# Kernel tuning notes

Hardware: AMD Instinct MI355X
Metric: run time of the kernel (lower is better)

Reference implementation:

```python
import jax, jax.numpy as jnp
import numpy as np

V, C, L, D = 16384, 16, 6, 64  # n_vars, max_clauses, max_variables, embedding_dim


def _normalize(x):
    # utils.normalize: L2-normalize along the feature axis
    return x / jnp.linalg.norm(x, axis=-1, keepdims=True)


def _rescombine(x, W1, b1, W2, b2):
    # ResidualCombine: normalize(sigmoid(layer1(x)) + layer2(x))
    h = jax.nn.sigmoid(x @ W1 + b1) + x @ W2 + b2
    return _normalize(h)


def setup_inputs() -> dict:
    key = jax.random.key(0)
    ks = jax.random.split(key, 14)
    s = 0.05
    variables = jax.random.normal(ks[0], (V, D), jnp.float32)
    # literal variable indices; slot 0 of every clause is the owning variable i
    lits = jax.random.randint(ks[1], (V, C, L), 0, V)
    lits = lits.at[:, :, 0].set(jnp.arange(V)[:, None])
    neg_mask = jax.random.bernoulli(ks[2], 0.5, (V, C, L))
    # literal validity: at least 2 literals per clause, slot 0 always valid
    nvar = jax.random.randint(ks[3], (V, C), 2, L + 1)
    var_valid = jnp.arange(L)[None, None, :] < nvar[:, :, None]
    # clause validity: at least 1 clause per variable
    nclause = jax.random.randint(ks[4], (V,), 1, C + 1)
    clause_valid = jnp.arange(C)[None, :] < nclause[:, None]
    # params
    Wn = jax.random.normal(ks[5], (D, D), jnp.float32) * s
    bn = jnp.zeros((D,), jnp.float32)
    f = jax.random.normal(ks[6], (D,), jnp.float32)
    false_emb = f / jnp.linalg.norm(f)  # Embedding(1, D, max_norm=1.0)
    W1v = jax.random.normal(ks[7], (L * D, D), jnp.float32) * s
    b1v = jnp.zeros((D,), jnp.float32)
    W2v = jax.random.normal(ks[8], (L * D, D), jnp.float32) * s
    b2v = jnp.zeros((D,), jnp.float32)
    W1c = jax.random.normal(ks[9], (C * D, D), jnp.float32) * s
    b1c = jnp.zeros((D,), jnp.float32)
    W2c = jax.random.normal(ks[10], (C * D, D), jnp.float32) * s
    b2c = jnp.zeros((D,), jnp.float32)
    return dict(variables=variables, lits=lits, neg_mask=neg_mask, var_valid=var_valid,
                clause_valid=clause_valid, Wn=Wn, bn=bn, false_emb=false_emb,
                W1v=W1v, b1v=b1v, W2v=W2v, b2v=b2v, W1c=W1c, b1c=b1c, W2c=W2c, b2c=b2c)


def reference(variables, lits, neg_mask, var_valid, clause_valid,
              Wn, bn, false_emb, W1v, b1v, W2v, b2v, W1c, b1c, W2c, b2c):
    # gather literal embeddings: [V, C, L, D]
    g = variables[lits]
    # negation linear for negative literals
    v = jnp.where(neg_mask[..., None], g @ Wn + bn, g)
    # pad invalid literal slots with the 'false' embedding
    v = jnp.where(var_valid[..., None], v, false_emb)
    # variable_combiner over flattened [L*D]
    clause_emb = _rescombine(v.reshape(V, C, L * D), W1v, b1v, W2v, b2v)  # [V, C, D]
    # pad missing clauses with 'true' = negation(false)
    true_emb = false_emb @ Wn + bn
    clause_emb = jnp.where(clause_valid[..., None], clause_emb, true_emb)
    # clause_combiner over flattened [C*D]
    out = _rescombine(clause_emb.reshape(V, C * D), W1c, b1c, W2c, b2c)  # [V, D]
    # variables with no clauses pass through unchanged
    has_clauses = clause_valid.any(axis=-1)
    return jnp.where(has_clauses[:, None], out, variables)
```

## Files before the change

### kernel.cpp

```cpp
#include <hip/hip_runtime.h>
#include <hip/hip_bf16.h>

#define NV 16384
#define NC 16
#define NL 6
#define ND 64

typedef unsigned short u16;
typedef unsigned int u32;
typedef __attribute__((ext_vector_type(8))) short short8;
typedef __attribute__((ext_vector_type(4))) unsigned short u16x4;
typedef __attribute__((ext_vector_type(4))) int i32x4;
typedef __attribute__((ext_vector_type(4))) float f32x4;

#define PB_BN  0
#define PB_FE  64
#define PB_B1V 128
#define PB_B2V 192
#define PB_B1C 256
#define PB_B2C 320
#define U_BVS   896
#define U_BCS   50048
#define U_BN    181120
#define U_VARSB 185216
#define U_NEGB  1233856
#define U_FIDX  2282496

__device__ __forceinline__ float ldbf(const u16* p, int i) {
  return __uint_as_float(((u32)p[i]) << 16);
}
__device__ __forceinline__ u16 f2b(float f) {
  u32 x = __float_as_uint(f);
  return (u16)((x + 0x7FFF + ((x >> 16) & 1)) >> 16);
}
__device__ __forceinline__ int ldmask(const void* p, int i, int bdt) {
  return bdt ? (int)((const signed char*)p)[i] : ((const int*)p)[i];
}
__device__ __forceinline__ int ldmask_nt(const void* p, int i, int bdt) {
  return bdt ? (int)__builtin_nontemporal_load((const signed char*)p + i)
             : __builtin_nontemporal_load((const int*)p + i);
}
__device__ __forceinline__ float ldf(const void* p, int i, int fdt) {
  return fdt ? ldbf((const u16*)p, i) : ((const float*)p)[i];
}
__device__ __forceinline__ void gll16(const u16* g, u16* l) {
  __builtin_amdgcn_global_load_lds(
      (const __attribute__((address_space(1))) u32*)(g),
      (__attribute__((address_space(3))) u32*)(l), 16, 0, 0);
}

__global__ __launch_bounds__(256) void k_prep(
    const void* vars, const int* __restrict__ lits, const void* negm, const void* vval,
    const void* Wn, const void* bn, const void* femb,
    const void* W1v, const void* b1v, const void* W2v, const void* b2v,
    const void* W1c, const void* b1c, const void* W2c, const void* b2c,
    int* flags, float* pbuf, u16* wsB) {
  __shared__ int s_cnt[4], s_big[4];
  __shared__ u16 wn[64 * 72];
  const int t = threadIdx.x;
  {
    const u32 w = ((const u32*)vars)[t];
    const u32 e = (w >> 7) & 0xFF;
    const unsigned long long bal = __ballot(e >= 0x6E && e <= 0x8E);
    const u32 bw = ((const u32*)vval)[t];
    const unsigned long long bb = __ballot(bw > 1u);
    if ((t & 63) == 0) { s_cnt[t >> 6] = __popcll(bal); s_big[t >> 6] = (bb != 0ull); }
  }
  __syncthreads();
  const int fdt = (s_cnt[0] + s_cnt[1] + s_cnt[2] + s_cnt[3]) >= 192;
  const int bdt = (s_big[0] | s_big[1] | s_big[2] | s_big[3]);
  const int bid = blockIdx.x;

  if (bid == 0) {
    if (t == 0) { flags[0] = fdt; flags[1] = bdt; }
    if (t < 64) {
      const void* src[6] = {bn, femb, b1v, b2v, b1c, b2c};
      const int off[6] = {PB_BN, PB_FE, PB_B1V, PB_B2V, PB_B1C, PB_B2C};
      for (int j = 0; j < 6; j++) pbuf[off[j] + t] = ldf(src[j], t, fdt);
      wsB[U_VARSB + NV * 64 + t] = fdt ? ((const u16*)femb)[t] : f2b(((const float*)femb)[t]);
    }
  } else if (bid < 25) {
    const int c = (bid - 1) * 256 + t;
    const int ln = c & 63, nt = (c >> 6) & 7, ks = c >> 9;
    const int n = nt * 16 + (ln & 15);
    const void* src = (n < 64) ? W1v : W2v;
    const int kb = ks * 32 + (ln >> 4) * 8, n6 = n & 63;
    u16 o[8];
#pragma unroll
    for (int j = 0; j < 8; j++) o[j] = f2b(ldf(src, (kb + j) * 64 + n6, fdt));
    *(short8*)(wsB + U_BVS + c * 8) = *(short8*)o;
  } else if (bid < 89) {
    const int c = (bid - 25) * 256 + t;
    const int ln = c & 63, nt = (c >> 6) & 7, ks = c >> 9;
    const int n = nt * 16 + (ln & 15);
    const void* src = (n < 64) ? W1c : W2c;
    const int kb = ks * 32 + (ln >> 4) * 8, n6 = n & 63;
    u16 o[8];
#pragma unroll
    for (int j = 0; j < 8; j++) o[j] = f2b(ldf(src, (kb + j) * 64 + n6, fdt));
    *(short8*)(wsB + U_BCS + c * 8) = *(short8*)o;
  } else if (bid < 601) {
    const int c8 = (bid - 89) * 256 + t;
    u16 o[8];
    if (fdt) {
      *(short8*)o = ((const short8*)vars)[c8];
    } else {
      const float* f = (const float*)vars + c8 * 8;
#pragma unroll
      for (int j = 0; j < 8; j++) o[j] = f2b(f[j]);
    }
    *(short8*)(wsB + U_VARSB + c8 * 8) = *(short8*)o;
  } else if (bid < 1369) {
    const int i0 = ((bid - 601) * 256 + t) * 8;
    const i32x4 l0 = __builtin_nontemporal_load((const i32x4*)((const int*)lits + i0));
    const i32x4 l1 = __builtin_nontemporal_load((const i32x4*)((const int*)lits + i0) + 1);
    int nm[8], vv[8];
    if (bdt) {
      const unsigned long long nmq =
          __builtin_nontemporal_load((const unsigned long long*)((const signed char*)negm + i0));
      const unsigned long long vvq =
          __builtin_nontemporal_load((const unsigned long long*)((const signed char*)vval + i0));
#pragma unroll
      for (int j = 0; j < 8; j++) {
        nm[j] = (int)((nmq >> (8 * j)) & 0xFF);
        vv[j] = (int)((vvq >> (8 * j)) & 0xFF);
      }
    } else {
      const i32x4 n0 = __builtin_nontemporal_load((const i32x4*)((const int*)negm + i0));
      const i32x4 n1 = __builtin_nontemporal_load((const i32x4*)((const int*)negm + i0) + 1);
      const i32x4 v0 = __builtin_nontemporal_load((const i32x4*)((const int*)vval + i0));
      const i32x4 v1 = __builtin_nontemporal_load((const i32x4*)((const int*)vval + i0) + 1);
#pragma unroll
      for (int j = 0; j < 4; j++) {
        nm[j] = n0[j]; nm[4 + j] = n1[j];
        vv[j] = v0[j]; vv[4 + j] = v1[j];
      }
    }
    u16 o[8];
#pragma unroll
    for (int j = 0; j < 8; j++) {
      const int idx = (j < 4) ? l0[j] : l1[j - 4];
      o[j] = (u16)(vv[j] ? (idx + (nm[j] ? (NV + 1) : 0)) : NV);
    }
    __builtin_nontemporal_store(*(short8*)o, (short8*)(wsB + U_FIDX + i0));
  } else {
    const int nb = bid - 1369;
    for (int e = t; e < 4096; e += 256) {
      const int k = e >> 6, n = e & 63;
      wn[n * 72 + k] = f2b(ldf(Wn, e, fdt));
    }
    __syncthreads();
    const int lane = t & 63, wv = t >> 6;
    const int col = lane & 15, quad = lane >> 4, q8 = quad * 8;
    const int rowbase = nb * 64 + wv * 16;
    f32x4 acc[4];
#pragma unroll
    for (int nt = 0; nt < 4; nt++) acc[nt] = (f32x4){0.f, 0.f, 0.f, 0.f};
    const int arow = min(rowbase + col, NV);
#pragma unroll
    for (int ks = 0; ks < 2; ks++) {
      short8 a;
      if (fdt) {
        const u16* ap = (arow == NV) ? (const u16*)femb : (const u16*)vars + arow * 64;
        a = *(const short8*)(ap + ks * 32 + q8);
      } else {
        const float* ap = (arow == NV) ? (const float*)femb : (const float*)vars + arow * 64;
        const f32x4 f0 = *(const f32x4*)(ap + ks * 32 + q8);
        const f32x4 f1 = *(const f32x4*)(ap + ks * 32 + q8 + 4);
#pragma unroll
        for (int j = 0; j < 4; j++) { a[j] = (short)f2b(f0[j]); a[4 + j] = (short)f2b(f1[j]); }
      }
#pragma unroll
      for (int nt = 0; nt < 4; nt++) {
        const short8 b = *(const short8*)(&wn[(nt * 16 + col) * 72 + ks * 32 + q8]);
        acc[nt] = __builtin_amdgcn_mfma_f32_16x16x32_bf16(a, b, acc[nt], 0, 0, 0);
      }
    }
#pragma unroll
    for (int reg = 0; reg < 4; reg++) {
      const int r = rowbase + quad * 4 + reg;
      if (r <= NV) {
#pragma unroll
        for (int nt = 0; nt < 4; nt++) {
          const int d = nt * 16 + col;
          wsB[U_NEGB + r * 64 + d] = f2b(acc[nt][reg] + ldf(bn, d, fdt));
        }
      }
    }
  }
}

__global__ __launch_bounds__(256, 2) void k_main(
    const void* __restrict__ vars, const void* __restrict__ cval,
    const float* __restrict__ pbuf, const int* __restrict__ flags,
    const u16* __restrict__ wsB, void* __restrict__ outv) {
  __shared__ __align__(16) u16 smem[24576];
  __shared__ float ps[16][4];
  __shared__ int hcS[16];

  const int tid = threadIdx.x, lane = tid & 63, wv = tid >> 6;
  const int col = lane & 15, quad = lane >> 4, q8 = quad * 8;
  const int fdt = flags[0], bdt = flags[1];
  const int vbase = (blockIdx.x * 4 + wv) * 4;
  const int v0 = blockIdx.x * 16;

  u32 r2_[4][3];
#pragma unroll
  for (int v4 = 0; v4 < 4; v4++)
#pragma unroll
    for (int i = 0; i < 3; i++)
      r2_[v4][i] = __builtin_nontemporal_load(
          (const u32*)(wsB + U_FIDX + (vbase + v4) * 96 + col * 6 + i * 2));

  const int cv = ldmask_nt(cval, vbase * 16 + lane, bdt);
  const unsigned long long bal = __ballot(cv != 0);
  if (lane < 4) hcS[wv * 4 + lane] = ((bal >> (lane * 16)) & 0xFFFFull) != 0;

  f32x4 acc[4][8];
#pragma unroll
  for (int v4 = 0; v4 < 4; v4++)
#pragma unroll
    for (int nt = 0; nt < 8; nt++) acc[v4][nt] = (f32x4){0.f, 0.f, 0.f, 0.f};

#pragma unroll
  for (int j = 0; j < 6; j++) {
    const int cl = wv * 6 + j;
    gll16(wsB + U_BVS + cl * 512 + lane * 8, &smem[cl * 512]);
  }
  short8 a_[3][4];
#pragma unroll
  for (int v4 = 0; v4 < 4; v4++) {
    const int idx = (int)(r2_[v4][0] & 0xFFFFu);
    a_[0][v4] = *(const short8*)(wsB + U_VARSB + idx * 64 + q8);
    a_[1][v4] = *(const short8*)(wsB + U_VARSB + idx * 64 + 32 + q8);
  }
  __syncthreads();

  for (int q = 0; q < 4; q++) {
    if (q < 3) {
#pragma unroll
      for (int j = 0; j < 6; j++) {
        const int cl = wv * 6 + j;
        gll16(wsB + U_BVS + (q + 1) * 12288 + cl * 512 + lane * 8,
              &smem[((q + 1) & 1) * 12288 + cl * 512]);
      }
    }
#pragma unroll
    for (int ksl = 0; ksl < 3; ksl++) {
      const int gk = q * 3 + ksl;
      const int gn = gk + 2;
      const int sf = (ksl + 2) % 3;
      if (gn < 12) {
        const int goff = (gn & 1) * 32 + q8;
        const int pi = gn >> 2, ph = (gn >> 1) & 1;
#pragma unroll
        for (int v4 = 0; v4 < 4; v4++) {
          const int idx = (int)((r2_[v4][pi] >> (ph * 16)) & 0xFFFFu);
          a_[sf][v4] = *(const short8*)(wsB + U_VARSB + idx * 64 + goff);
        }
      }
      __builtin_amdgcn_s_setprio(1);
#pragma unroll
      for (int nt = 0; nt < 8; nt++) {
        const short8 b = *(const short8*)(&smem[(q & 1) * 12288 + (ksl * 8 + nt) * 512 + lane * 8]);
#pragma unroll
        for (int v4 = 0; v4 < 4; v4++)
          acc[v4][nt] = __builtin_amdgcn_mfma_f32_16x16x32_bf16(a_[ksl][v4], b, acc[v4][nt], 0, 0, 0);
      }
      __builtin_amdgcn_s_setprio(0);
    }
    if (q < 3) __syncthreads();
  }
  __syncthreads();

  {
    float b1l[4], b2l[4], truel[4];
#pragma unroll
    for (int nt = 0; nt < 4; nt++) {
      const int d = nt * 16 + col;
      b1l[nt] = pbuf[PB_B1V + d];
      b2l[nt] = pbuf[PB_B2V + d];
      truel[nt] = ldbf(wsB, U_NEGB + NV * 64 + d);
    }
#pragma unroll
    for (int v4 = 0; v4 < 4; v4++) {
      const u32 vmask = (u32)((bal >> (v4 * 16)) & 0xFFFFull);
      const int vloc = wv * 4 + v4;
#pragma unroll
      for (int reg = 0; reg < 4; reg++) {
        const int c = quad * 4 + reg;
        float hh[4], ss = 0.f;
#pragma unroll
        for (int nt = 0; nt < 4; nt++) {
          hh[nt] = 1.0f / (1.0f + __expf(-(acc[v4][nt][reg] + b1l[nt]))) + acc[v4][nt + 4][reg] + b2l[nt];
          ss += hh[nt] * hh[nt];
        }
        ss += __shfl_xor(ss, 1, 64); ss += __shfl_xor(ss, 2, 64);
        ss += __shfl_xor(ss, 4, 64); ss += __shfl_xor(ss, 8, 64);
        const float sc = 1.0f / sqrtf(ss);
        const int valid = (vmask >> c) & 1;
#pragma unroll
        for (int nt = 0; nt < 4; nt++) {
          const float o = valid ? hh[nt] * sc : truel[nt];
          const int l2 = (nt * 2 + (col >> 3)) & 3;
          smem[(c * 2 + (nt >> 1)) * 512 + (l2 * 16 + vloc) * 8 + (col & 7)] = f2b(o);
        }
      }
    }
  }
  __syncthreads();

  f32x4 acc1 = (f32x4){0.f, 0.f, 0.f, 0.f}, acc2 = (f32x4){0.f, 0.f, 0.f, 0.f};
#pragma unroll 8
  for (int ks = 0; ks < 32; ks++) {
    const short8 a = *(const short8*)(&smem[ks * 512 + lane * 8]);
    const short8 b1 = *(const short8*)(wsB + U_BCS + (ks * 8 + wv) * 512 + lane * 8);
    const short8 b2 = *(const short8*)(wsB + U_BCS + (ks * 8 + wv + 4) * 512 + lane * 8);
    acc1 = __builtin_amdgcn_mfma_f32_16x16x32_bf16(a, b1, acc1, 0, 0, 0);
    acc2 = __builtin_amdgcn_mfma_f32_16x16x32_bf16(a, b2, acc2, 0, 0, 0);
  }

  const int d = wv * 16 + col;
  const float b1c_d = pbuf[PB_B1C + d], b2c_d = pbuf[PB_B2C + d];
  float h[4];
#pragma unroll
  for (int reg = 0; reg < 4; reg++) {
    h[reg] = 1.0f / (1.0f + __expf(-(acc1[reg] + b1c_d))) + acc2[reg] + b2c_d;
    float ssp = h[reg] * h[reg];
    ssp += __shfl_xor(ssp, 1, 64); ssp += __shfl_xor(ssp, 2, 64);
    ssp += __shfl_xor(ssp, 4, 64); ssp += __shfl_xor(ssp, 8, 64);
    if (col == 0) ps[quad * 4 + reg][wv] = ssp;
  }
  __syncthreads();
#pragma unroll
  for (int reg = 0; reg < 4; reg++) {
    const int r = quad * 4 + reg;
    const float tot = ps[r][0] + ps[r][1] + ps[r][2] + ps[r][3];
    float o = h[reg] * (1.0f / sqrtf(tot));
    const int oi = (v0 + r) * 64 + d;
    if (hcS[r]) {
      if (fdt) __builtin_nontemporal_store(f2b(o), &((u16*)outv)[oi]);
      else __builtin_nontemporal_store(o, &((float*)outv)[oi]);
    } else {
      if (fdt) __builtin_nontemporal_store(
          __builtin_nontemporal_load(&((const u16*)vars)[oi]), &((u16*)outv)[oi]);
      else __builtin_nontemporal_store(
          __builtin_nontemporal_load(&((const float*)vars)[oi]), &((float*)outv)[oi]);
    }
  }
}

extern "C" void kernel_launch(void* const* d_in, const int* in_sizes, int n_in,
                              void* d_out, int out_size, void* d_ws, size_t ws_size,
                              hipStream_t stream) {
  const void* vars = d_in[0];
  const int* lits = (const int*)d_in[1];
  const void* negm = d_in[2];
  const void* vval = d_in[3];
  const void* cvalid = d_in[4];
  const void* Wn = d_in[5];
  const void* bn = d_in[6];
  const void* femb = d_in[7];
  const void* W1v = d_in[8];
  const void* b1v = d_in[9];
  const void* W2v = d_in[10];
  const void* b2v = d_in[11];
  const void* W1c = d_in[12];
  const void* b1c = d_in[13];
  const void* W2c = d_in[14];
  const void* b2c = d_in[15];

  int* flags = (int*)d_ws;
  float* pbuf = (float*)((char*)d_ws + 256);
  u16* wsB = (u16*)d_ws;

  k_prep<<<1626, 256, 0, stream>>>(vars, lits, negm, vval, Wn, bn, femb,
                                   W1v, b1v, W2v, b2v, W1c, b1c, W2c, b2c,
                                   flags, pbuf, wsB);
  k_main<<<NV / 16, 256, 0, stream>>>(vars, cvalid, pbuf, flags, wsB, d_out);
}
```

Baseline: 153.5 us.

## Permute clause-weight K order to vectorize LDS stores; split second GEMM accumulators

Clause-combiner weights are stored with a permuted K ordering. This lets each lane write its four normalized clause-embedding outputs as one 4-wide LDS store instead of four scalar scattered stores. The second GEMM loop is split into two halves with separate accumulators, which breaks the MFMA dependency chain. The setprio hints around the first GEMM are removed. These changes aim to cut LDS store count and MFMA latency stalls, and they depend on the weight permutation exactly matching the new LDS layout.

Result: slower. 161.3 us (+5.1%).

```diff
diff --git a/kernel.cpp b/kernel.cpp
--- a/kernel.cpp
+++ b/kernel.cpp
@@ -9,6 +9,7 @@
 typedef unsigned short u16;
 typedef unsigned int u32;
 typedef __attribute__((ext_vector_type(8))) short short8;
+typedef __attribute__((ext_vector_type(4))) short short4e;
 typedef __attribute__((ext_vector_type(4))) unsigned short u16x4;
 typedef __attribute__((ext_vector_type(4))) int i32x4;
 typedef __attribute__((ext_vector_type(4))) float f32x4;
@@ -97,7 +98,11 @@
     const int kb = ks * 32 + (ln >> 4) * 8, n6 = n & 63;
     u16 o[8];
 #pragma unroll
-    for (int j = 0; j < 8; j++) o[j] = f2b(ldf(src, (kb + j) * 64 + n6, fdt));
+    for (int j = 0; j < 8; j++) {
+      const int kp = kb + j;
+      const int knat = ((kp >> 6) << 6) + ((kp & 3) << 4) + ((kp >> 2) & 15);
+      o[j] = f2b(ldf(src, knat * 64 + n6, fdt));
+    }
     *(short8*)(wsB + U_BCS + c * 8) = *(short8*)o;
   } else if (bid < 601) {
     const int c8 = (bid - 89) * 256 + t;
@@ -259,7 +264,6 @@
           a_[sf][v4] = *(const short8*)(wsB + U_VARSB + idx * 64 + goff);
         }
       }
-      __builtin_amdgcn_s_setprio(1);
 #pragma unroll
       for (int nt = 0; nt < 8; nt++) {
         const short8 b = *(const short8*)(&smem[(q & 1) * 12288 + (ksl * 8 + nt) * 512 + lane * 8]);
@@ -267,7 +271,6 @@
         for (int v4 = 0; v4 < 4; v4++)
           acc[v4][nt] = __builtin_amdgcn_mfma_f32_16x16x32_bf16(a_[ksl][v4], b, acc[v4][nt], 0, 0, 0);
       }
-      __builtin_amdgcn_s_setprio(0);
     }
     if (q < 3) __syncthreads();
   }
@@ -299,26 +302,36 @@
         ss += __shfl_xor(ss, 4, 64); ss += __shfl_xor(ss, 8, 64);
         const float sc = 1.0f / sqrtf(ss);
         const int valid = (vmask >> c) & 1;
-#pragma unroll
-        for (int nt = 0; nt < 4; nt++) {
-          const float o = valid ? hh[nt] * sc : truel[nt];
-          const int l2 = (nt * 2 + (col >> 3)) & 3;
-          smem[(c * 2 + (nt >> 1)) * 512 + (l2 * 16 + vloc) * 8 + (col & 7)] = f2b(o);
-        }
-      }
-    }
-  }
-  __syncthreads();
-
-  f32x4 acc1 = (f32x4){0.f, 0.f, 0.f, 0.f}, acc2 = (f32x4){0.f, 0.f, 0.f, 0.f};
+        u16 o4[4];
+#pragma unroll
+        for (int nt = 0; nt < 4; nt++)
+          o4[nt] = f2b(valid ? hh[nt] * sc : truel[nt]);
+        const int L = ((col & 7) >> 1) * 16 + vloc;
+        *(short4e*)(&smem[(c * 2 + (col >> 3)) * 512 + L * 8 + (col & 1) * 4]) =
+            *(short4e*)o4;
+      }
+    }
+  }
+  __syncthreads();
+
+  f32x4 p1a = (f32x4){0.f, 0.f, 0.f, 0.f}, p1b = p1a, p2a = p1a, p2b = p1a;
 #pragma unroll 8
-  for (int ks = 0; ks < 32; ks++) {
+  for (int ks = 0; ks < 16; ks++) {
     const short8 a = *(const short8*)(&smem[ks * 512 + lane * 8]);
     const short8 b1 = *(const short8*)(wsB + U_BCS + (ks * 8 + wv) * 512 + lane * 8);
     const short8 b2 = *(const short8*)(wsB + U_BCS + (ks * 8 + wv + 4) * 512 + lane * 8);
-    acc1 = __builtin_amdgcn_mfma_f32_16x16x32_bf16(a, b1, acc1, 0, 0, 0);
-    acc2 = __builtin_amdgcn_mfma_f32_16x16x32_bf16(a, b2, acc2, 0, 0, 0);
-  }
+    p1a = __builtin_amdgcn_mfma_f32_16x16x32_bf16(a, b1, p1a, 0, 0, 0);
+    p2a = __builtin_amdgcn_mfma_f32_16x16x32_bf16(a, b2, p2a, 0, 0, 0);
+  }
+#pragma unroll 8
+  for (int ks = 16; ks < 32; ks++) {
+    const short8 a = *(const short8*)(&smem[ks * 512 + lane * 8]);
+    const short8 b1 = *(const short8*)(wsB + U_BCS + (ks * 8 + wv) * 512 + lane * 8);
+    const short8 b2 = *(const short8*)(wsB + U_BCS + (ks * 8 + wv + 4) * 512 + lane * 8);
+    p1b = __builtin_amdgcn_mfma_f32_16x16x32_bf16(a, b1, p1b, 0, 0, 0);
+    p2b = __builtin_amdgcn_mfma_f32_16x16x32_bf16(a, b2, p2b, 0, 0, 0);
+  }
+  const f32x4 acc1 = p1a + p1b, acc2 = p2a + p2b;
 
   const int d = wv * 16 + col;
   const float b1c_d = pbuf[PB_B1C + d], b2c_d = pbuf[PB_B2C + d];
```

## Double k_main block to 512 threads with split-K clause combiner

Applied to the files above, without the earlier changes.

k_main now launches 8 waves per block instead of 4. In stage 1 each wave handles 2 variables instead of 4, which halves per-wave accumulator registers. Stage 2 splits the K loop across two wave groups and reduces the partial sums through shared memory. The aim is more waves in flight to hide the gather latency, at the cost of an extra barrier and more shared-memory traffic.

Result: no change. 152.3 us (-0.8%).

```diff
diff --git a/kernel.cpp b/kernel.cpp
--- a/kernel.cpp
+++ b/kernel.cpp
@@ -190,7 +190,7 @@
   }
 }
 
-__global__ __launch_bounds__(256, 2) void k_main(
+__global__ __launch_bounds__(512, 4) void k_main(
     const void* __restrict__ vars, const void* __restrict__ cval,
     const float* __restrict__ pbuf, const int* __restrict__ flags,
     const u16* __restrict__ wsB, void* __restrict__ outv) {
@@ -201,35 +201,35 @@
   const int tid = threadIdx.x, lane = tid & 63, wv = tid >> 6;
   const int col = lane & 15, quad = lane >> 4, q8 = quad * 8;
   const int fdt = flags[0], bdt = flags[1];
-  const int vbase = (blockIdx.x * 4 + wv) * 4;
+  const int vbase = blockIdx.x * 16 + wv * 2;
   const int v0 = blockIdx.x * 16;
 
-  u32 r2_[4][3];
-#pragma unroll
-  for (int v4 = 0; v4 < 4; v4++)
+  u32 r2_[2][3];
+#pragma unroll
+  for (int v4 = 0; v4 < 2; v4++)
 #pragma unroll
     for (int i = 0; i < 3; i++)
       r2_[v4][i] = __builtin_nontemporal_load(
           (const u32*)(wsB + U_FIDX + (vbase + v4) * 96 + col * 6 + i * 2));
 
-  const int cv = ldmask_nt(cval, vbase * 16 + lane, bdt);
+  const int cv = ldmask_nt(cval, vbase * 16 + (lane & 31), bdt);
   const unsigned long long bal = __ballot(cv != 0);
-  if (lane < 4) hcS[wv * 4 + lane] = ((bal >> (lane * 16)) & 0xFFFFull) != 0;
-
-  f32x4 acc[4][8];
-#pragma unroll
-  for (int v4 = 0; v4 < 4; v4++)
+  if (lane < 2) hcS[wv * 2 + lane] = ((bal >> (lane * 16)) & 0xFFFFull) != 0;
+
+  f32x4 acc[2][8];
+#pragma unroll
+  for (int v4 = 0; v4 < 2; v4++)
 #pragma unroll
     for (int nt = 0; nt < 8; nt++) acc[v4][nt] = (f32x4){0.f, 0.f, 0.f, 0.f};
 
 #pragma unroll
-  for (int j = 0; j < 6; j++) {
-    const int cl = wv * 6 + j;
+  for (int j = 0; j < 3; j++) {
+    const int cl = wv * 3 + j;
     gll16(wsB + U_BVS + cl * 512 + lane * 8, &smem[cl * 512]);
   }
-  short8 a_[3][4];
-#pragma unroll
-  for (int v4 = 0; v4 < 4; v4++) {
+  short8 a_[3][2];
+#pragma unroll
+  for (int v4 = 0; v4 < 2; v4++) {
     const int idx = (int)(r2_[v4][0] & 0xFFFFu);
     a_[0][v4] = *(const short8*)(wsB + U_VARSB + idx * 64 + q8);
     a_[1][v4] = *(const short8*)(wsB + U_VARSB + idx * 64 + 32 + q8);
@@ -239,8 +239,8 @@
   for (int q = 0; q < 4; q++) {
     if (q < 3) {
 #pragma unroll
-      for (int j = 0; j < 6; j++) {
-        const int cl = wv * 6 + j;
+      for (int j = 0; j < 3; j++) {
+        const int cl = wv * 3 + j;
         gll16(wsB + U_BVS + (q + 1) * 12288 + cl * 512 + lane * 8,
               &smem[((q + 1) & 1) * 12288 + cl * 512]);
       }
@@ -254,7 +254,7 @@
         const int goff = (gn & 1) * 32 + q8;
         const int pi = gn >> 2, ph = (gn >> 1) & 1;
 #pragma unroll
-        for (int v4 = 0; v4 < 4; v4++) {
+        for (int v4 = 0; v4 < 2; v4++) {
           const int idx = (int)((r2_[v4][pi] >> (ph * 16)) & 0xFFFFu);
           a_[sf][v4] = *(const short8*)(wsB + U_VARSB + idx * 64 + goff);
         }
@@ -264,7 +264,7 @@
       for (int nt = 0; nt < 8; nt++) {
         const short8 b = *(const short8*)(&smem[(q & 1) * 12288 + (ksl * 8 + nt) * 512 + lane * 8]);
 #pragma unroll
-        for (int v4 = 0; v4 < 4; v4++)
+        for (int v4 = 0; v4 < 2; v4++)
           acc[v4][nt] = __builtin_amdgcn_mfma_f32_16x16x32_bf16(a_[ksl][v4], b, acc[v4][nt], 0, 0, 0);
       }
       __builtin_amdgcn_s_setprio(0);
@@ -283,9 +283,9 @@
       truel[nt] = ldbf(wsB, U_NEGB + NV * 64 + d);
     }
 #pragma unroll
-    for (int v4 = 0; v4 < 4; v4++) {
+    for (int v4 = 0; v4 < 2; v4++) {
       const u32 vmask = (u32)((bal >> (v4 * 16)) & 0xFFFFull);
-      const int vloc = wv * 4 + v4;
+      const int vloc = wv * 2 + v4;
 #pragma unroll
       for (int reg = 0; reg < 4; reg++) {
         const int c = quad * 4 + reg;
@@ -310,42 +310,58 @@
   }
   __syncthreads();
 
+  const int g = wv & 3, kh = wv >> 2;
   f32x4 acc1 = (f32x4){0.f, 0.f, 0.f, 0.f}, acc2 = (f32x4){0.f, 0.f, 0.f, 0.f};
 #pragma unroll 8
-  for (int ks = 0; ks < 32; ks++) {
+  for (int ks = kh * 16; ks < kh * 16 + 16; ks++) {
     const short8 a = *(const short8*)(&smem[ks * 512 + lane * 8]);
-    const short8 b1 = *(const short8*)(wsB + U_BCS + (ks * 8 + wv) * 512 + lane * 8);
-    const short8 b2 = *(const short8*)(wsB + U_BCS + (ks * 8 + wv + 4) * 512 + lane * 8);
+    const short8 b1 = *(const short8*)(wsB + U_BCS + (ks * 8 + g) * 512 + lane * 8);
+    const short8 b2 = *(const short8*)(wsB + U_BCS + (ks * 8 + g + 4) * 512 + lane * 8);
     acc1 = __builtin_amdgcn_mfma_f32_16x16x32_bf16(a, b1, acc1, 0, 0, 0);
     acc2 = __builtin_amdgcn_mfma_f32_16x16x32_bf16(a, b2, acc2, 0, 0, 0);
   }
-
-  const int d = wv * 16 + col;
-  const float b1c_d = pbuf[PB_B1C + d], b2c_d = pbuf[PB_B2C + d];
+  float* red = (float*)(smem + 16384);
+  if (kh) {
+    const int base = (g * 64 + lane) * 8;
+    *(f32x4*)(red + base) = acc1;
+    *(f32x4*)(red + base + 4) = acc2;
+  }
+  __syncthreads();
+
   float h[4];
-#pragma unroll
-  for (int reg = 0; reg < 4; reg++) {
-    h[reg] = 1.0f / (1.0f + __expf(-(acc1[reg] + b1c_d))) + acc2[reg] + b2c_d;
-    float ssp = h[reg] * h[reg];
-    ssp += __shfl_xor(ssp, 1, 64); ssp += __shfl_xor(ssp, 2, 64);
-    ssp += __shfl_xor(ssp, 4, 64); ssp += __shfl_xor(ssp, 8, 64);
-    if (col == 0) ps[quad * 4 + reg][wv] = ssp;
-  }
-  __syncthreads();
-#pragma unroll
-  for (int reg = 0; reg < 4; reg++) {
-    const int r = quad * 4 + reg;
-    const float tot = ps[r][0] + ps[r][1] + ps[r][2] + ps[r][3];
-    float o = h[reg] * (1.0f / sqrtf(tot));
-    const int oi = (v0 + r) * 64 + d;
-    if (hcS[r]) {
-      if (fdt) __builtin_nontemporal_store(f2b(o), &((u16*)outv)[oi]);
-      else __builtin_nontemporal_store(o, &((float*)outv)[oi]);
-    } else {
-      if (fdt) __builtin_nontemporal_store(
-          __builtin_nontemporal_load(&((const u16*)vars)[oi]), &((u16*)outv)[oi]);
-      else __builtin_nontemporal_store(
-          __builtin_nontemporal_load(&((const float*)vars)[oi]), &((float*)outv)[oi]);
+  if (!kh) {
+    const int base = (g * 64 + lane) * 8;
+    acc1 += *(const f32x4*)(red + base);
+    acc2 += *(const f32x4*)(red + base + 4);
+    const int d = g * 16 + col;
+    const float b1c_d = pbuf[PB_B1C + d], b2c_d = pbuf[PB_B2C + d];
+#pragma unroll
+    for (int reg = 0; reg < 4; reg++) {
+      h[reg] = 1.0f / (1.0f + __expf(-(acc1[reg] + b1c_d))) + acc2[reg] + b2c_d;
+      float ssp = h[reg] * h[reg];
+      ssp += __shfl_xor(ssp, 1, 64); ssp += __shfl_xor(ssp, 2, 64);
+      ssp += __shfl_xor(ssp, 4, 64); ssp += __shfl_xor(ssp, 8, 64);
+      if (col == 0) ps[quad * 4 + reg][g] = ssp;
+    }
+  }
+  __syncthreads();
+  if (!kh) {
+    const int d = g * 16 + col;
+#pragma unroll
+    for (int reg = 0; reg < 4; reg++) {
+      const int r = quad * 4 + reg;
+      const float tot = ps[r][0] + ps[r][1] + ps[r][2] + ps[r][3];
+      float o = h[reg] * (1.0f / sqrtf(tot));
+      const int oi = (v0 + r) * 64 + d;
+      if (hcS[r]) {
+        if (fdt) __builtin_nontemporal_store(f2b(o), &((u16*)outv)[oi]);
+        else __builtin_nontemporal_store(o, &((float*)outv)[oi]);
+      } else {
+        if (fdt) __builtin_nontemporal_store(
+            __builtin_nontemporal_load(&((const u16*)vars)[oi]), &((u16*)outv)[oi]);
+        else __builtin_nontemporal_store(
+            __builtin_nontemporal_load(&((const float*)vars)[oi]), &((float*)outv)[oi]);
+      }
     }
   }
 }
@@ -377,5 +393,5 @@
   k_prep<<<1626, 256, 0, stream>>>(vars, lits, negm, vval, Wn, bn, femb,
                                    W1v, b1v, W2v, b2v, W1c, b1c, W2c, b2c,
                                    flags, pbuf, wsB);
-  k_main<<<NV / 16, 256, 0, stream>>>(vars, cvalid, pbuf, flags, wsB, d_out);
-}
+  k_main<<<NV / 16, 512, 0, stream>>>(vars, cvalid, pbuf, flags, wsB, d_out);
+}
```
